# Optimization experiments

Measured on AMD Instinct MI355X. Metric: run time of the kernel, lower is better.

Reference implementation:

```python
import jax, jax.numpy as jnp
import numpy as np

B, S, C = 8, 2048, 512

def setup_inputs() -> dict:
    key = jax.random.key(0)
    ks = jax.random.split(key, 7)
    s = 1.0 / np.sqrt(C)
    return {
        "x": jax.random.normal(ks[0], (B, S, C), dtype=jnp.float32),
        "Wq": jax.random.uniform(ks[1], (C, C), jnp.float32, -s, s),
        "bq": jax.random.uniform(ks[2], (C,), jnp.float32, -s, s),
        "Wk": jax.random.uniform(ks[3], (C, C), jnp.float32, -s, s),
        "bk": jax.random.uniform(ks[4], (C,), jnp.float32, -s, s),
        "Wv": jax.random.uniform(ks[5], (C, C), jnp.float32, -s, s),
        "bv": jax.random.uniform(ks[6], (C,), jnp.float32, -s, s),
    }

def reference(x, Wq, bq, Wk, bk, Wv, bv):
    # Linear projections (torch Linear: x @ W.T + b)
    q = jnp.einsum('bsc,dc->bsd', x, Wq) + bq
    k = jnp.einsum('bsc,dc->bsd', x, Wk) + bk
    v = jnp.einsum('bsc,dc->bsd', x, Wv) + bv
    # NOTE: original code computes dk but never scales by 1/sqrt(dk)
    scores = jnp.einsum('bqd,bkd->bqk', q, k)          # [B,S,S]
    attn = jax.nn.softmax(scores, axis=-1)
    out = jnp.einsum('bqk,bkd->bqd', attn, v)
    return out + x
```

## Files before the change

kernel.cpp:

```cpp
#include <hip/hip_runtime.h>
#include <hip/hip_bf16.h>


typedef __bf16 bf16_t;
typedef bf16_t bf16x8 __attribute__((ext_vector_type(8)));
typedef float floatx4 __attribute__((ext_vector_type(4)));

#define MFMA16(a, b, c) __builtin_amdgcn_mfma_f32_16x16x32_bf16((a), (b), (c), 0, 0, 0)
#define FLASH_LDS 136704

__device__ __forceinline__ void gload16(const void* g, void* l) {
    __builtin_amdgcn_global_load_lds((const __attribute__((address_space(1))) void*)g,
                                     (__attribute__((address_space(3))) void*)l, 16, 0, 0);
}

__device__ __forceinline__ float wave16_sum(float v) {
    v += __shfl_xor(v, 1);
    v += __shfl_xor(v, 2);
    v += __shfl_xor(v, 4);
    v += __shfl_xor(v, 8);
    return v;
}

__global__ void convert_in(const float* __restrict__ X,
                           const float* __restrict__ Wq, const float* __restrict__ Wk,
                           const float* __restrict__ Wv, const float* __restrict__ bq,
                           const float* __restrict__ bk, const float* __restrict__ bv,
                           bf16_t* __restrict__ Xb, bf16_t* __restrict__ Wb,
                           float* __restrict__ biasc) {
    int bid = blockIdx.x, tid = threadIdx.x;
    if (bid < 4096) {
        size_t e0 = ((size_t)bid * 256 + tid) * 8;
        float4 f0 = *(const float4*)(X + e0);
        float4 f1 = *(const float4*)(X + e0 + 4);
        bf16x8 o;
        o[0] = (bf16_t)f0.x; o[1] = (bf16_t)f0.y; o[2] = (bf16_t)f0.z; o[3] = (bf16_t)f0.w;
        o[4] = (bf16_t)f1.x; o[5] = (bf16_t)f1.y; o[6] = (bf16_t)f1.z; o[7] = (bf16_t)f1.w;
        *(bf16x8*)(Xb + e0) = o;
    } else {
        int idx = (bid - 4096) * 256 + tid;
        int e0 = idx * 4;
        int row = e0 >> 9, c = e0 & 511;
        const float* src;
        if (row < 512)       src = Wq + row * 512;
        else if (row < 1024) src = Wk + (row - 512) * 512;
        else                 src = Wv + (row - 1024) * 512;
        float4 v = *(const float4*)(src + c);
        Wb[e0 + 0] = (bf16_t)v.x;
        Wb[e0 + 1] = (bf16_t)v.y;
        Wb[e0 + 2] = (bf16_t)v.z;
        Wb[e0 + 3] = (bf16_t)v.w;
        if (idx < 1536) {
            float b;
            if (idx < 512)       b = bq[idx];
            else if (idx < 1024) b = bk[idx - 512];
            else                 b = bv[idx - 1024];
            biasc[idx] = b;
        }
    }
}

__global__ __launch_bounds__(256, 2)
void qkv_gemm(const bf16_t* __restrict__ Xb, const bf16_t* __restrict__ Wb,
              const float* __restrict__ biasc, bf16_t* __restrict__ Q,
              bf16_t* __restrict__ K, bf16_t* __restrict__ Vt) {
    __shared__ int4 smem4[2560];
    char* As = (char*)smem4;
    char* Bs = (char*)smem4 + 16384;
    char* Vtile = (char*)smem4;

    const int tid = threadIdx.x;
    const int l = tid & 63, w = tid >> 6;
    const int lane16 = l & 15, lq = l >> 4;
    const int klo = lane16 & 7;
    const int m0 = (blockIdx.x & 127) << 7;
    const int n0 = (blockIdx.x >> 7) << 7;
    const int wm = (w >> 1) << 6, wn = (w & 1) << 6;
    const int srow = l >> 3;
    const int sc8 = (l & 7) ^ srow;

    floatx4 acc[4][4];
#pragma unroll
    for (int a = 0; a < 4; ++a)
#pragma unroll
        for (int bb = 0; bb < 4; ++bb) acc[a][bb] = (floatx4){0.f, 0.f, 0.f, 0.f};

    for (int it = 0; it < 8; ++it) {
        __syncthreads();
#pragma unroll
        for (int j = 0; j < 4; ++j) {
            int seg = j * 4 + w;
            int row = seg * 8 + srow;
            gload16(Xb + (size_t)(m0 + row) * 512 + it * 64 + sc8 * 8, As + seg * 1024);
            gload16(Wb + (size_t)(n0 + row) * 512 + it * 64 + sc8 * 8, Bs + seg * 1024);
        }
        __syncthreads();
#pragma unroll
        for (int kst = 0; kst < 2; ++kst) {
            bf16x8 afr[4], bfr[4];
#pragma unroll
            for (int mt = 0; mt < 4; ++mt)
                afr[mt] = *(const bf16x8*)(As + (wm + mt * 16 + lane16) * 128 +
                                           ((kst * 4 + lq) ^ klo) * 16);
#pragma unroll
            for (int nt = 0; nt < 4; ++nt)
                bfr[nt] = *(const bf16x8*)(Bs + (wn + nt * 16 + lane16) * 128 +
                                           ((kst * 4 + lq) ^ klo) * 16);
#pragma unroll
            for (int mt = 0; mt < 4; ++mt)
#pragma unroll
                for (int nt = 0; nt < 4; ++nt)
                    acc[mt][nt] = MFMA16(afr[mt], bfr[nt], acc[mt][nt]);
        }
    }

    float bias_v[4];
#pragma unroll
    for (int nt = 0; nt < 4; ++nt) bias_v[nt] = biasc[n0 + wn + nt * 16 + lane16];

    if (n0 < 1024) {
        bf16_t* Dst = (n0 < 512) ? Q : K;
        const int coff = (n0 < 512 ? n0 : n0 - 512) + wn;
#pragma unroll
        for (int mt = 0; mt < 4; ++mt)
#pragma unroll
            for (int nt = 0; nt < 4; ++nt)
#pragma unroll
                for (int i = 0; i < 4; ++i) {
                    int rowM = m0 + wm + mt * 16 + lq * 4 + i;
                    Dst[(size_t)rowM * 512 + coff + nt * 16 + lane16] =
                        (bf16_t)(acc[mt][nt][i] + bias_v[nt]);
                }
    } else {
        __syncthreads();
#pragma unroll
        for (int mt = 0; mt < 4; ++mt)
#pragma unroll
            for (int nt = 0; nt < 4; ++nt)
#pragma unroll
                for (int i = 0; i < 4; ++i) {
                    int dl = wn + nt * 16 + lane16;
                    int sl = wm + mt * 16 + lq * 4 + i;
                    *(bf16_t*)(Vtile + dl * 264 + sl * 2) =
                        (bf16_t)(acc[mt][nt][i] + bias_v[nt]);
                }
        __syncthreads();
        const int bb = m0 >> 11, s0 = m0 & 2047, dbase = n0 - 1024;
#pragma unroll
        for (int j = 0; j < 8; ++j) {
            int slot = j * 256 + tid;
            int dd = slot >> 4, c = slot & 15;
            *(int4*)(Vt + (size_t)(bb * 512 + dbase + dd) * 2048 + s0 + c * 8) =
                *(const int4*)(Vtile + dd * 264 + c * 16);
        }
    }
}

__global__ __launch_bounds__(512, 2)
void flash_attn_v7(const bf16_t* __restrict__ Q, const bf16_t* __restrict__ K,
                   const bf16_t* __restrict__ Vt, const float* __restrict__ X,
                   float* __restrict__ Out) {
    extern __shared__ char smem[];
    char* Ps = smem + 131072;
    float* lpart = (float*)(smem + 136192);

    const int tid = threadIdx.x;
    const int l = tid & 63, w = tid >> 6;
    const int lane16 = l & 15, lq = l >> 4;
    const int qg = w >> 1, h = w & 1;
    const int dbase = w << 6;
    const int b = blockIdx.x & 7;
    const int q0 = (blockIdx.x >> 3) << 6;

    const bf16_t* Kbase = K + (size_t)b * 2048 * 512;
    const bf16_t* Vbase = Vt + (size_t)b * 512 * 2048;

    const int dl_v = ((l >> 3) << 1) | ((l & 7) >> 2);
    const int vc   = (l & 3) ^ ((l >> 3) & 3);

    auto stageK = [&](int kt, char* Kb) {
#pragma unroll
        for (int j = 0; j < 4; ++j) {
            int seg = j * 8 + w;
            int c = (l & ~7) | ((l & 7) ^ (seg & 7));
            gload16(Kbase + ((size_t)kt * 32 + seg) * 512 + c * 8, Kb + seg * 1024);
        }
    };
    auto stageV = [&](int kt, char* Vb) {
        const bf16_t* Vsrc = Vbase + kt * 32;
#pragma unroll
        for (int j = 0; j < 4; ++j) {
            int seg = j * 8 + w;
            int d = seg * 16 + dl_v;
            gload16(Vsrc + (size_t)d * 2048 + vc * 8, Vb + seg * 1024);
        }
    };

    stageK(0, smem);
    stageV(0, smem + 65536);

    bf16x8 qf[16];
    const bf16_t* Qrow = Q + (size_t)(b * 2048 + q0 + qg * 16 + lane16) * 512 + lq * 8;
#pragma unroll
    for (int kst = 0; kst < 16; ++kst) qf[kst] = *(const bf16x8*)(Qrow + kst * 32);

    floatx4 o[16];
#pragma unroll
    for (int t = 0; t < 16; ++t) o[t] = (floatx4){0.f, 0.f, 0.f, 0.f};
    float lsum[4] = {0.f, 0.f, 0.f, 0.f};
    const float L2E = 1.4426950408889634f;
    const int key = h * 16 + lane16;

    __syncthreads();

    for (int kt = 0; kt < 64; ++kt) {
        char* Kcur = smem + (kt & 1) * 32768;
        char* Vcur = smem + 65536 + (kt & 1) * 32768;

        if (kt < 63) {
            stageK(kt + 1, smem + ((kt + 1) & 1) * 32768);
            stageV(kt + 1, smem + 65536 + ((kt + 1) & 1) * 32768);
        }

        floatx4 sc = (floatx4){0.f, 0.f, 0.f, 0.f};
#pragma unroll
        for (int kst = 0; kst < 16; ++kst) {
            int i0 = kst * 4 + lq;
            int p0 = (i0 & ~7) | ((i0 & 7) ^ (key & 7));
            bf16x8 kb = *(const bf16x8*)(Kcur + key * 1024 + p0 * 16);
            sc = MFMA16(qf[kst], kb, sc);
        }

#pragma unroll
        for (int i = 0; i < 4; ++i) {
            int row = qg * 16 + lq * 4 + i;
            float p = __builtin_exp2f(sc[i] * L2E);
            lsum[i] += p;
            *(bf16_t*)(Ps + row * 80 + key * 2) = (bf16_t)p;
        }

        asm volatile("s_waitcnt lgkmcnt(0)\n\ts_barrier" ::: "memory");
        __builtin_amdgcn_sched_barrier(0);

        bf16x8 pa[4], vb[4];
#pragma unroll
        for (int qgi = 0; qgi < 4; ++qgi)
            pa[qgi] = *(const bf16x8*)(Ps + (qgi * 16 + lane16) * 80 + lq * 16);
#pragma unroll
        for (int dg = 0; dg < 4; ++dg) {
            int d = dbase + dg * 16 + lane16;
            int slot = (d & 1) * 4 + (lq ^ ((d >> 1) & 3));
            vb[dg] = *(const bf16x8*)(Vcur + (d >> 1) * 128 + slot * 16);
        }
#pragma unroll
        for (int dg = 0; dg < 4; ++dg)
#pragma unroll
            for (int qgi = 0; qgi < 4; ++qgi)
                o[qgi * 4 + dg] = MFMA16(pa[qgi], vb[dg], o[qgi * 4 + dg]);

        __syncthreads();
    }

#pragma unroll
    for (int i = 0; i < 4; ++i) {
        float s = wave16_sum(lsum[i]);
        if (lane16 == 0) lpart[(qg * 16 + lq * 4 + i) * 2 + h] = s;
    }
    __syncthreads();

#pragma unroll
    for (int qgi = 0; qgi < 4; ++qgi) {
        float rinv[4];
#pragma unroll
        for (int i = 0; i < 4; ++i) {
            int row = qgi * 16 + lq * 4 + i;
            rinv[i] = 1.0f / (lpart[row * 2] + lpart[row * 2 + 1]);
        }
#pragma unroll
        for (int dg = 0; dg < 4; ++dg) {
            int d = dbase + dg * 16 + lane16;
#pragma unroll
            for (int i = 0; i < 4; ++i) {
                int row = q0 + qgi * 16 + lq * 4 + i;
                size_t g = (size_t)(b * 2048 + row) * 512 + d;
                Out[g] = o[qgi * 4 + dg][i] * rinv[i] + X[g];
            }
        }
    }
}

extern "C" void kernel_launch(void* const* d_in, const int* in_sizes, int n_in,
                              void* d_out, int out_size, void* d_ws, size_t ws_size,
                              hipStream_t stream) {
    const float* x  = (const float*)d_in[0];
    const float* Wq = (const float*)d_in[1];
    const float* bq = (const float*)d_in[2];
    const float* Wk = (const float*)d_in[3];
    const float* bk = (const float*)d_in[4];
    const float* Wv = (const float*)d_in[5];
    const float* bv = (const float*)d_in[6];
    float* out = (float*)d_out;
    char* ws = (char*)d_ws;

    bf16_t* Wb    = (bf16_t*)(ws);
    float*  biasc = (float*)(ws + 1572864);
    bf16_t* Xb    = (bf16_t*)(ws + 1579008);
    bf16_t* Qb    = (bf16_t*)(ws + 18356224);
    bf16_t* Kb    = (bf16_t*)(ws + 35133440);
    bf16_t* Vt    = (bf16_t*)(ws + 51910656);

    convert_in<<<4864, 256, 0, stream>>>(x, Wq, Wk, Wv, bq, bk, bv, Xb, Wb, biasc);
    qkv_gemm<<<1536, 256, 0, stream>>>(Xb, Wb, biasc, Qb, Kb, Vt);

    hipFuncSetAttribute(reinterpret_cast<const void*>(flash_attn_v7),
                        hipFuncAttributeMaxDynamicSharedMemorySize, FLASH_LDS);
    flash_attn_v7<<<256, 512, FLASH_LDS, stream>>>(Qb, Kb, Vt, x, out);
}
```

Baseline: 221.6 us.

## Software-pipeline QK^T of next tile with PV of current tile

Restructures the flash attention loop so the score MFMA and exp for key tile kt+1 run alongside the PV MFMA for tile kt. P is double-buffered in LDS and K is prefetched two tiles ahead. This removes the mid-iteration barrier between softmax writes and PV reads. The cost is extra LDS and a prologue step.

```diff
diff --git a/kernel.cpp b/kernel.cpp
--- a/kernel.cpp
+++ b/kernel.cpp
@@ -7,7 +7,7 @@
 typedef float floatx4 __attribute__((ext_vector_type(4)));
 
 #define MFMA16(a, b, c) __builtin_amdgcn_mfma_f32_16x16x32_bf16((a), (b), (c), 0, 0, 0)
-#define FLASH_LDS 136704
+#define FLASH_LDS 141824
 
 __device__ __forceinline__ void gload16(const void* g, void* l) {
     __builtin_amdgcn_global_load_lds((const __attribute__((address_space(1))) void*)g,
@@ -157,12 +157,11 @@
 }
 
 __global__ __launch_bounds__(512, 2)
-void flash_attn_v7(const bf16_t* __restrict__ Q, const bf16_t* __restrict__ K,
+void flash_attn_v8(const bf16_t* __restrict__ Q, const bf16_t* __restrict__ K,
                    const bf16_t* __restrict__ Vt, const float* __restrict__ X,
                    float* __restrict__ Out) {
     extern __shared__ char smem[];
-    char* Ps = smem + 131072;
-    float* lpart = (float*)(smem + 136192);
+    float* lpart = (float*)(smem + 141312);
 
     const int tid = threadIdx.x;
     const int l = tid & 63, w = tid >> 6;
@@ -210,53 +209,75 @@
     float lsum[4] = {0.f, 0.f, 0.f, 0.f};
     const float L2E = 1.4426950408889634f;
     const int key = h * 16 + lane16;
+    const int prow = qg * 16 + lq * 4;
 
     __syncthreads();
 
-    for (int kt = 0; kt < 64; ++kt) {
-        char* Kcur = smem + (kt & 1) * 32768;
-        char* Vcur = smem + 65536 + (kt & 1) * 32768;
-
-        if (kt < 63) {
-            stageK(kt + 1, smem + ((kt + 1) & 1) * 32768);
-            stageV(kt + 1, smem + 65536 + ((kt + 1) & 1) * 32768);
-        }
-
+    stageK(1, smem + 32768);
+    {
         floatx4 sc = (floatx4){0.f, 0.f, 0.f, 0.f};
 #pragma unroll
         for (int kst = 0; kst < 16; ++kst) {
             int i0 = kst * 4 + lq;
             int p0 = (i0 & ~7) | ((i0 & 7) ^ (key & 7));
-            bf16x8 kb = *(const bf16x8*)(Kcur + key * 1024 + p0 * 16);
+            bf16x8 kb = *(const bf16x8*)(smem + key * 1024 + p0 * 16);
             sc = MFMA16(qf[kst], kb, sc);
         }
-
 #pragma unroll
         for (int i = 0; i < 4; ++i) {
-            int row = qg * 16 + lq * 4 + i;
             float p = __builtin_exp2f(sc[i] * L2E);
             lsum[i] += p;
-            *(bf16_t*)(Ps + row * 80 + key * 2) = (bf16_t)p;
-        }
-
-        asm volatile("s_waitcnt lgkmcnt(0)\n\ts_barrier" ::: "memory");
-        __builtin_amdgcn_sched_barrier(0);
-
-        bf16x8 pa[4], vb[4];
-#pragma unroll
-        for (int qgi = 0; qgi < 4; ++qgi)
-            pa[qgi] = *(const bf16x8*)(Ps + (qgi * 16 + lane16) * 80 + lq * 16);
-#pragma unroll
-        for (int dg = 0; dg < 4; ++dg) {
-            int d = dbase + dg * 16 + lane16;
-            int slot = (d & 1) * 4 + (lq ^ ((d >> 1) & 3));
-            vb[dg] = *(const bf16x8*)(Vcur + (d >> 1) * 128 + slot * 16);
-        }
-#pragma unroll
-        for (int dg = 0; dg < 4; ++dg)
+            *(bf16_t*)(smem + 131072 + (prow + i) * 80 + key * 2) = (bf16_t)p;
+        }
+    }
+    __syncthreads();
+
+    for (int kt = 0; kt < 64; ++kt) {
+        char* Knext = smem + ((kt + 1) & 1) * 32768;
+        char* Vcur  = smem + 65536 + (kt & 1) * 32768;
+        char* Pcur  = smem + 131072 + (kt & 1) * 5120;
+        char* Pnext = smem + 131072 + ((kt + 1) & 1) * 5120;
+
+        if (kt < 62) stageK(kt + 2, smem + (kt & 1) * 32768);
+        if (kt < 63) stageV(kt + 1, smem + 65536 + ((kt + 1) & 1) * 32768);
+
+        floatx4 sc = (floatx4){0.f, 0.f, 0.f, 0.f};
+        if (kt < 63) {
+#pragma unroll
+            for (int kst = 0; kst < 16; ++kst) {
+                int i0 = kst * 4 + lq;
+                int p0 = (i0 & ~7) | ((i0 & 7) ^ (key & 7));
+                bf16x8 kb = *(const bf16x8*)(Knext + key * 1024 + p0 * 16);
+                sc = MFMA16(qf[kst], kb, sc);
+            }
+        }
+
+        {
+            bf16x8 pa[4], vb[4];
 #pragma unroll
             for (int qgi = 0; qgi < 4; ++qgi)
-                o[qgi * 4 + dg] = MFMA16(pa[qgi], vb[dg], o[qgi * 4 + dg]);
+                pa[qgi] = *(const bf16x8*)(Pcur + (qgi * 16 + lane16) * 80 + lq * 16);
+#pragma unroll
+            for (int dg = 0; dg < 4; ++dg) {
+                int d = dbase + dg * 16 + lane16;
+                int slot = (d & 1) * 4 + (lq ^ ((d >> 1) & 3));
+                vb[dg] = *(const bf16x8*)(Vcur + (d >> 1) * 128 + slot * 16);
+            }
+#pragma unroll
+            for (int dg = 0; dg < 4; ++dg)
+#pragma unroll
+                for (int qgi = 0; qgi < 4; ++qgi)
+                    o[qgi * 4 + dg] = MFMA16(pa[qgi], vb[dg], o[qgi * 4 + dg]);
+        }
+
+        if (kt < 63) {
+#pragma unroll
+            for (int i = 0; i < 4; ++i) {
+                float p = __builtin_exp2f(sc[i] * L2E);
+                lsum[i] += p;
+                *(bf16_t*)(Pnext + (prow + i) * 80 + key * 2) = (bf16_t)p;
+            }
+        }
 
         __syncthreads();
     }
@@ -264,7 +285,7 @@
 #pragma unroll
     for (int i = 0; i < 4; ++i) {
         float s = wave16_sum(lsum[i]);
-        if (lane16 == 0) lpart[(qg * 16 + lq * 4 + i) * 2 + h] = s;
+        if (lane16 == 0) lpart[(prow + i) * 2 + h] = s;
     }
     __syncthreads();
 
@@ -312,7 +333,7 @@
     convert_in<<<4864, 256, 0, stream>>>(x, Wq, Wk, Wv, bq, bk, bv, Xb, Wb, biasc);
     qkv_gemm<<<1536, 256, 0, stream>>>(Xb, Wb, biasc, Qb, Kb, Vt);
 
-    hipFuncSetAttribute(reinterpret_cast<const void*>(flash_attn_v7),
+    hipFuncSetAttribute(reinterpret_cast<const void*>(flash_attn_v8),
                         hipFuncAttributeMaxDynamicSharedMemorySize, FLASH_LDS);
-    flash_attn_v7<<<256, 512, FLASH_LDS, stream>>>(Qb, Kb, Vt, x, out);
-}
+    flash_attn_v8<<<256, 512, FLASH_LDS, stream>>>(Qb, Kb, Vt, x, out);
+}
```

Measured after the change: 228.6 us. 1.03x slower.

## Halve query tile, single-buffer K/V, and raise occupancy to four blocks per CU

Applied to the files above, without the earlier changes.

The attention kernel now handles 32 query rows per block instead of 64 and launches 512 blocks. K and V are single-buffered in LDS, so LDS per block drops by half and launch bounds allow four blocks per CU. Only four of the eight waves compute scores; V loading is interleaved with score computation and the next K load is issued after the barrier. The aim is more resident blocks and fewer registers to hide latency, at the cost of losing the double-buffer prefetch, adding an extra barrier per tile, leaving half the waves idle during QK, and reading K/V twice as often overall.

```diff
diff --git a/kernel.cpp b/kernel.cpp
--- a/kernel.cpp
+++ b/kernel.cpp
@@ -7,7 +7,7 @@
 typedef float floatx4 __attribute__((ext_vector_type(4)));
 
 #define MFMA16(a, b, c) __builtin_amdgcn_mfma_f32_16x16x32_bf16((a), (b), (c), 0, 0, 0)
-#define FLASH_LDS 136704
+#define FLASH_LDS 68352
 
 __device__ __forceinline__ void gload16(const void* g, void* l) {
     __builtin_amdgcn_global_load_lds((const __attribute__((address_space(1))) void*)g,
@@ -156,13 +156,15 @@
     }
 }
 
-__global__ __launch_bounds__(512, 2)
-void flash_attn_v7(const bf16_t* __restrict__ Q, const bf16_t* __restrict__ K,
-                   const bf16_t* __restrict__ Vt, const float* __restrict__ X,
-                   float* __restrict__ Out) {
+__global__ __launch_bounds__(512, 4)
+void flash_attn_v10(const bf16_t* __restrict__ Q, const bf16_t* __restrict__ K,
+                    const bf16_t* __restrict__ Vt, const float* __restrict__ X,
+                    float* __restrict__ Out) {
     extern __shared__ char smem[];
-    char* Ps = smem + 131072;
-    float* lpart = (float*)(smem + 136192);
+    char* Ks = smem;
+    char* Vs = smem + 32768;
+    char* Ps = smem + 65536;
+    float* lpart = (float*)(smem + 68096);
 
     const int tid = threadIdx.x;
     const int l = tid & 63, w = tid >> 6;
@@ -170,7 +172,7 @@
     const int qg = w >> 1, h = w & 1;
     const int dbase = w << 6;
     const int b = blockIdx.x & 7;
-    const int q0 = (blockIdx.x >> 3) << 6;
+    const int q0 = (blockIdx.x >> 3) << 5;
 
     const bf16_t* Kbase = K + (size_t)b * 2048 * 512;
     const bf16_t* Vbase = Vt + (size_t)b * 512 * 2048;
@@ -178,98 +180,98 @@
     const int dl_v = ((l >> 3) << 1) | ((l & 7) >> 2);
     const int vc   = (l & 3) ^ ((l >> 3) & 3);
 
-    auto stageK = [&](int kt, char* Kb) {
+    auto stageK = [&](int kt) {
 #pragma unroll
         for (int j = 0; j < 4; ++j) {
             int seg = j * 8 + w;
             int c = (l & ~7) | ((l & 7) ^ (seg & 7));
-            gload16(Kbase + ((size_t)kt * 32 + seg) * 512 + c * 8, Kb + seg * 1024);
+            gload16(Kbase + ((size_t)kt * 32 + seg) * 512 + c * 8, Ks + seg * 1024);
         }
     };
-    auto stageV = [&](int kt, char* Vb) {
+    auto stageV = [&](int kt) {
         const bf16_t* Vsrc = Vbase + kt * 32;
 #pragma unroll
         for (int j = 0; j < 4; ++j) {
             int seg = j * 8 + w;
             int d = seg * 16 + dl_v;
-            gload16(Vsrc + (size_t)d * 2048 + vc * 8, Vb + seg * 1024);
+            gload16(Vsrc + (size_t)d * 2048 + vc * 8, Vs + seg * 1024);
         }
     };
 
-    stageK(0, smem);
-    stageV(0, smem + 65536);
+    stageK(0);
 
     bf16x8 qf[16];
-    const bf16_t* Qrow = Q + (size_t)(b * 2048 + q0 + qg * 16 + lane16) * 512 + lq * 8;
-#pragma unroll
-    for (int kst = 0; kst < 16; ++kst) qf[kst] = *(const bf16x8*)(Qrow + kst * 32);
-
-    floatx4 o[16];
-#pragma unroll
-    for (int t = 0; t < 16; ++t) o[t] = (floatx4){0.f, 0.f, 0.f, 0.f};
+    if (w < 4) {
+        const bf16_t* Qrow =
+            Q + (size_t)(b * 2048 + q0 + qg * 16 + lane16) * 512 + lq * 8;
+#pragma unroll
+        for (int kst = 0; kst < 16; ++kst) qf[kst] = *(const bf16x8*)(Qrow + kst * 32);
+    }
+
+    floatx4 o[8];
+#pragma unroll
+    for (int t = 0; t < 8; ++t) o[t] = (floatx4){0.f, 0.f, 0.f, 0.f};
     float lsum[4] = {0.f, 0.f, 0.f, 0.f};
     const float L2E = 1.4426950408889634f;
     const int key = h * 16 + lane16;
+    const int prow = qg * 16 + lq * 4;
 
     __syncthreads();
 
     for (int kt = 0; kt < 64; ++kt) {
-        char* Kcur = smem + (kt & 1) * 32768;
-        char* Vcur = smem + 65536 + (kt & 1) * 32768;
-
-        if (kt < 63) {
-            stageK(kt + 1, smem + ((kt + 1) & 1) * 32768);
-            stageV(kt + 1, smem + 65536 + ((kt + 1) & 1) * 32768);
-        }
-
-        floatx4 sc = (floatx4){0.f, 0.f, 0.f, 0.f};
-#pragma unroll
-        for (int kst = 0; kst < 16; ++kst) {
-            int i0 = kst * 4 + lq;
-            int p0 = (i0 & ~7) | ((i0 & 7) ^ (key & 7));
-            bf16x8 kb = *(const bf16x8*)(Kcur + key * 1024 + p0 * 16);
-            sc = MFMA16(qf[kst], kb, sc);
-        }
-
+        stageV(kt);
+
+        if (w < 4) {
+            floatx4 sc = (floatx4){0.f, 0.f, 0.f, 0.f};
+#pragma unroll
+            for (int kst = 0; kst < 16; ++kst) {
+                int i0 = kst * 4 + lq;
+                int p0 = (i0 & ~7) | ((i0 & 7) ^ (key & 7));
+                bf16x8 kb = *(const bf16x8*)(Ks + key * 1024 + p0 * 16);
+                sc = MFMA16(qf[kst], kb, sc);
+            }
+#pragma unroll
+            for (int i = 0; i < 4; ++i) {
+                float p = __builtin_exp2f(sc[i] * L2E);
+                lsum[i] += p;
+                *(bf16_t*)(Ps + (prow + i) * 80 + key * 2) = (bf16_t)p;
+            }
+        }
+        __syncthreads();
+
+        if (kt < 63) stageK(kt + 1);
+
+        {
+            bf16x8 pa[2], vb[4];
+#pragma unroll
+            for (int qgi = 0; qgi < 2; ++qgi)
+                pa[qgi] = *(const bf16x8*)(Ps + (qgi * 16 + lane16) * 80 + lq * 16);
+#pragma unroll
+            for (int dg = 0; dg < 4; ++dg) {
+                int d = dbase + dg * 16 + lane16;
+                int slot = (d & 1) * 4 + (lq ^ ((d >> 1) & 3));
+                vb[dg] = *(const bf16x8*)(Vs + (d >> 1) * 128 + slot * 16);
+            }
+#pragma unroll
+            for (int dg = 0; dg < 4; ++dg)
+#pragma unroll
+                for (int qgi = 0; qgi < 2; ++qgi)
+                    o[qgi * 4 + dg] = MFMA16(pa[qgi], vb[dg], o[qgi * 4 + dg]);
+        }
+        __syncthreads();
+    }
+
+    if (w < 4) {
 #pragma unroll
         for (int i = 0; i < 4; ++i) {
-            int row = qg * 16 + lq * 4 + i;
-            float p = __builtin_exp2f(sc[i] * L2E);
-            lsum[i] += p;
-            *(bf16_t*)(Ps + row * 80 + key * 2) = (bf16_t)p;
-        }
-
-        asm volatile("s_waitcnt lgkmcnt(0)\n\ts_barrier" ::: "memory");
-        __builtin_amdgcn_sched_barrier(0);
-
-        bf16x8 pa[4], vb[4];
-#pragma unroll
-        for (int qgi = 0; qgi < 4; ++qgi)
-            pa[qgi] = *(const bf16x8*)(Ps + (qgi * 16 + lane16) * 80 + lq * 16);
-#pragma unroll
-        for (int dg = 0; dg < 4; ++dg) {
-            int d = dbase + dg * 16 + lane16;
-            int slot = (d & 1) * 4 + (lq ^ ((d >> 1) & 3));
-            vb[dg] = *(const bf16x8*)(Vcur + (d >> 1) * 128 + slot * 16);
-        }
-#pragma unroll
-        for (int dg = 0; dg < 4; ++dg)
-#pragma unroll
-            for (int qgi = 0; qgi < 4; ++qgi)
-                o[qgi * 4 + dg] = MFMA16(pa[qgi], vb[dg], o[qgi * 4 + dg]);
-
-        __syncthreads();
-    }
-
-#pragma unroll
-    for (int i = 0; i < 4; ++i) {
-        float s = wave16_sum(lsum[i]);
-        if (lane16 == 0) lpart[(qg * 16 + lq * 4 + i) * 2 + h] = s;
+            float s = wave16_sum(lsum[i]);
+            if (lane16 == 0) lpart[(prow + i) * 2 + h] = s;
+        }
     }
     __syncthreads();
 
 #pragma unroll
-    for (int qgi = 0; qgi < 4; ++qgi) {
+    for (int qgi = 0; qgi < 2; ++qgi) {
         float rinv[4];
 #pragma unroll
         for (int i = 0; i < 4; ++i) {
@@ -312,7 +314,7 @@
     convert_in<<<4864, 256, 0, stream>>>(x, Wq, Wk, Wv, bq, bk, bv, Xb, Wb, biasc);
     qkv_gemm<<<1536, 256, 0, stream>>>(Xb, Wb, biasc, Qb, Kb, Vt);
 
-    hipFuncSetAttribute(reinterpret_cast<const void*>(flash_attn_v7),
+    hipFuncSetAttribute(reinterpret_cast<const void*>(flash_attn_v10),
                         hipFuncAttributeMaxDynamicSharedMemorySize, FLASH_LDS);
-    flash_attn_v7<<<256, 512, FLASH_LDS, stream>>>(Qb, Kb, Vt, x, out);
-}
+    flash_attn_v10<<<512, 512, FLASH_LDS, stream>>>(Qb, Kb, Vt, x, out);
+}
```

New measurement: 292.6 us. 32.1% more time.
